# Kernel tuning notes

Measured on AMD Instinct MI355X. Metric: run time of the kernel, lower is better.

Reference implementation:

```python
import jax, jax.numpy as jnp
import numpy as np

B, T, D, H, STRIDE, MLP = 2, 2048, 1024, 16, 8, 4096
HD = D // H
EPS = 1e-5


def _ln(x, g, b):
    m = x.mean(-1, keepdims=True)
    v = x.var(-1, keepdims=True)
    return (x - m) * jax.lax.rsqrt(v + EPS) * g + b


def setup_inputs() -> dict:
    key = jax.random.key(0)
    ks = jax.random.split(key, 6)
    s = lambda k, shape: (jax.random.normal(k, shape, jnp.float32) * 0.02)
    return {
        "x": jax.random.normal(ks[0], (B, T, D), jnp.float32),
        "w_in": s(ks[1], (3 * D, D)),   # torch in_proj_weight
        "b_in": jnp.zeros((3 * D,), jnp.float32),
        "w_out": s(ks[2], (D, D)),      # attn out_proj
        "b_out": jnp.zeros((D,), jnp.float32),
        "w1": s(ks[3], (MLP, D)),       # mlp first Linear (torch layout [out,in])
        "b1": jnp.zeros((MLP,), jnp.float32),
        "w2": s(ks[4], (D, MLP)),       # mlp second Linear
        "b2": jnp.zeros((D,), jnp.float32),
        "ln1_g": jnp.ones((D,), jnp.float32),
        "ln1_b": jnp.zeros((D,), jnp.float32),
        "ln2_g": jnp.ones((D,), jnp.float32),
        "ln2_b": jnp.zeros((D,), jnp.float32),
    }


def reference(x, w_in, b_in, w_out, b_out, w1, b1, w2, b2,
              ln1_g, ln1_b, ln2_g, ln2_b):
    Bs, Ts, Ds = x.shape
    xn = _ln(x, ln1_g, ln1_b)
    # fused qkv projection (torch Linear: y = x @ W.T + b)
    qkv = xn @ w_in.T + b_in                              # [B,T,3D]
    q, k, v = jnp.split(qkv, 3, axis=-1)
    to_heads = lambda t: t.reshape(Bs, Ts, H, HD).transpose(0, 2, 1, 3)
    q, k, v = to_heads(q), to_heads(k), to_heads(v)       # [B,H,T,hd]
    scores = jnp.einsum("bhqd,bhkd->bhqk", q, k) / jnp.sqrt(jnp.float32(HD))
    # mask: rows at multiples of STRIDE attend everywhere; others only to self
    idx = jnp.arange(Ts)
    allowed = ((idx % STRIDE) == 0)[:, None] | (idx[:, None] == idx[None, :])
    scores = jnp.where(allowed, scores, -jnp.inf)
    attn = jax.nn.softmax(scores, axis=-1)
    o = jnp.einsum("bhqk,bhkd->bhqd", attn, v)            # [B,H,T,hd]
    o = o.transpose(0, 2, 1, 3).reshape(Bs, Ts, Ds)
    o = o @ w_out.T + b_out
    x = x + o
    xn = _ln(x, ln2_g, ln2_b)
    h = jax.nn.gelu(xn @ w1.T + b1, approximate=False)    # torch nn.GELU default = exact
    x = x + (h @ w2.T + b2)
    return x
```

## Files before the change

### kernel.cpp

```cpp
#include <hip/hip_runtime.h>

#define D_ 1024
#define T_ 2048
#define B_ 2
#define H_ 16
#define MLP_ 4096
#define NTOK (B_*T_)
#define QG 256
#define L2E 1.44269504088896340736f

typedef float f32x4 __attribute__((ext_vector_type(4)));
typedef __bf16 bf16x8 __attribute__((ext_vector_type(8)));

__device__ __forceinline__ unsigned short f2bf(float f) {
  unsigned int u = __float_as_uint(f);
  u += 0x7fff + ((u >> 16) & 1);
  return (unsigned short)(u >> 16);
}

__device__ __forceinline__ float wave_sum(float v) {
  for (int o = 32; o > 0; o >>= 1) v += __shfl_down(v, o, 64);
  return v;
}

__device__ __forceinline__ void gload16(const unsigned short* g, unsigned short* l) {
  __builtin_amdgcn_global_load_lds(
      (const __attribute__((address_space(1))) void*)g,
      (__attribute__((address_space(3))) void*)l, 16, 0, 0);
}

__device__ __forceinline__ unsigned ldsoff(const void* p) {
  return (unsigned)(size_t)(const __attribute__((address_space(3))) void*)p;
}

__device__ __forceinline__ void agload16(const unsigned short* g, unsigned m0v) {
  unsigned su = __builtin_amdgcn_readfirstlane(m0v);
  asm volatile("s_mov_b32 m0, %0\n\t"
               "global_load_lds_dwordx4 %1, off"
               :: "s"(su), "v"(g) : "memory");
}

#define N4_WIN  786432
#define N4_WOUT 262144
#define N4_W1   1048576
#define N4_W2   1048576
#define NCASTB  12288
__global__ void castln_kernel(const float* __restrict__ w_in,
                              const float* __restrict__ w_out,
                              const float* __restrict__ w1,
                              const float* __restrict__ w2,
                              unsigned short* __restrict__ o_in,
                              unsigned short* __restrict__ o_out,
                              unsigned short* __restrict__ o1,
                              unsigned short* __restrict__ o2,
                              const float* __restrict__ x,
                              const float* __restrict__ g,
                              const float* __restrict__ b,
                              unsigned short* __restrict__ xn) {
  int blk = blockIdx.x;
  int tid = threadIdx.x;
  if (blk < NTOK) {
    int wave = tid >> 6, lane = tid & 63;
    float4 v = ((const float4*)(x + (size_t)blk * D_))[tid];
    float s  = v.x + v.y + v.z + v.w;
    float s2 = v.x*v.x + v.y*v.y + v.z*v.z + v.w*v.w;
    s = wave_sum(s); s2 = wave_sum(s2);
    __shared__ float r1[4], r2[4];
    if (lane == 0) { r1[wave] = s; r2[wave] = s2; }
    __syncthreads();
    float ts  = r1[0] + r1[1] + r1[2] + r1[3];
    float ts2 = r2[0] + r2[1] + r2[2] + r2[3];
    float mean = ts * (1.0f / D_);
    float var  = ts2 * (1.0f / D_) - mean * mean;
    float rs = rsqrtf(var + 1e-5f);
    float4 gv = ((const float4*)g)[tid];
    float4 bv = ((const float4*)b)[tid];
    ushort4 o;
    o.x = f2bf((v.x - mean) * rs * gv.x + bv.x);
    o.y = f2bf((v.y - mean) * rs * gv.y + bv.y);
    o.z = f2bf((v.z - mean) * rs * gv.z + bv.z);
    o.w = f2bf((v.w - mean) * rs * gv.w + bv.w);
    ((ushort4*)(xn + (size_t)blk * D_))[tid] = o;
  } else {
    int i = (blk - NTOK) * 256 + tid;
    const float* src; unsigned short* dst; int j = i;
    if (i < N4_WIN) { src = w_in; dst = o_in; }
    else if ((j -= N4_WIN) < N4_WOUT) { src = w_out; dst = o_out; }
    else if ((j -= N4_WOUT) < N4_W1) { src = w1; dst = o1; }
    else { j -= N4_W1; src = w2; dst = o2; }
    float4 v = ((const float4*)src)[j];
    ushort4 o;
    o.x = f2bf(v.x); o.y = f2bf(v.y); o.z = f2bf(v.z); o.w = f2bf(v.w);
    ((ushort4*)dst)[j] = o;
  }
}

__global__ void ln_kernel(const float* __restrict__ x, const float* __restrict__ g,
                          const float* __restrict__ b, unsigned short* __restrict__ out) {
  int row = blockIdx.x;
  int tid = threadIdx.x;
  int wave = tid >> 6, lane = tid & 63;
  float4 v = ((const float4*)(x + (size_t)row * D_))[tid];
  float s  = v.x + v.y + v.z + v.w;
  float s2 = v.x*v.x + v.y*v.y + v.z*v.z + v.w*v.w;
  s = wave_sum(s); s2 = wave_sum(s2);
  __shared__ float r1[4], r2[4];
  if (lane == 0) { r1[wave] = s; r2[wave] = s2; }
  __syncthreads();
  float ts  = r1[0] + r1[1] + r1[2] + r1[3];
  float ts2 = r2[0] + r2[1] + r2[2] + r2[3];
  float mean = ts * (1.0f / D_);
  float var  = ts2 * (1.0f / D_) - mean * mean;
  float rs = rsqrtf(var + 1e-5f);
  float4 gv = ((const float4*)g)[tid];
  float4 bv = ((const float4*)b)[tid];
  ushort4 o;
  o.x = f2bf((v.x - mean) * rs * gv.x + bv.x);
  o.y = f2bf((v.y - mean) * rs * gv.y + bv.y);
  o.z = f2bf((v.z - mean) * rs * gv.z + bv.z);
  o.w = f2bf((v.w - mean) * rs * gv.w + bv.w);
  ((ushort4*)(out + (size_t)row * D_))[tid] = o;
}

__global__ void reduce_ln_kernel(const float* __restrict__ part,
                                 const float* __restrict__ x,
                                 const float* __restrict__ bias,
                                 const float* __restrict__ g,
                                 const float* __restrict__ b,
                                 float* __restrict__ x1,
                                 unsigned short* __restrict__ xn2) {
  int row = blockIdx.x;
  int tid = threadIdx.x;
  int wave = tid >> 6, lane = tid & 63;
  size_t base = (size_t)row * (D_ / 4) + tid;
  float4 v = ((const float4*)x)[base];
  float4 bo = ((const float4*)bias)[tid];
  v.x += bo.x; v.y += bo.y; v.z += bo.z; v.w += bo.w;
#pragma unroll
  for (int c = 0; c < 2; ++c) {
    float4 p = ((const float4*)part)[(size_t)c * (NTOK * (D_ / 4)) + base];
    v.x += p.x; v.y += p.y; v.z += p.z; v.w += p.w;
  }
  ((float4*)x1)[base] = v;
  float s  = v.x + v.y + v.z + v.w;
  float s2 = v.x*v.x + v.y*v.y + v.z*v.z + v.w*v.w;
  s = wave_sum(s); s2 = wave_sum(s2);
  __shared__ float r1[4], r2[4];
  if (lane == 0) { r1[wave] = s; r2[wave] = s2; }
  __syncthreads();
  float ts  = r1[0] + r1[1] + r1[2] + r1[3];
  float ts2 = r2[0] + r2[1] + r2[2] + r2[3];
  float mean = ts * (1.0f / D_);
  float var  = ts2 * (1.0f / D_) - mean * mean;
  float rs = rsqrtf(var + 1e-5f);
  float4 gv = ((const float4*)g)[tid];
  float4 bv = ((const float4*)b)[tid];
  ushort4 o;
  o.x = f2bf((v.x - mean) * rs * gv.x + bv.x);
  o.y = f2bf((v.y - mean) * rs * gv.y + bv.y);
  o.z = f2bf((v.z - mean) * rs * gv.z + bv.z);
  o.w = f2bf((v.w - mean) * rs * gv.w + bv.w);
  ((ushort4*)xn2)[base] = o;
}

__global__ void reduce_out_kernel(const float* __restrict__ part,
                                  const float* __restrict__ x1,
                                  const float* __restrict__ bias,
                                  float* __restrict__ out) {
  int i = blockIdx.x * 256 + threadIdx.x;
  float4 v = ((const float4*)x1)[i];
  float4 bo = ((const float4*)bias)[i & (D_ / 4 - 1)];
  v.x += bo.x; v.y += bo.y; v.z += bo.z; v.w += bo.w;
#pragma unroll
  for (int c = 0; c < 2; ++c) {
    float4 p = ((const float4*)part)[(size_t)c * (NTOK * (D_ / 4)) + i];
    v.x += p.x; v.y += p.y; v.z += p.z; v.w += p.w;
  }
  ((float4*)out)[i] = v;
}

template<int EPI>
__global__ __launch_bounds__(256)
void gemm128p_kernel(const unsigned short* __restrict__ A, int LDA,
                     const unsigned short* __restrict__ Bm, int LDB,
                     void* __restrict__ Cv, size_t sC, int LDC,
                     const float* __restrict__ bias,
                     unsigned short* __restrict__ aux1,
                     unsigned short* __restrict__ aux2,
                     int K, int nx, int ny) {
  __shared__ __align__(16) unsigned short As[2 * 8192];
  __shared__ __align__(16) unsigned short Bs[2 * 8192];
  const int flat = blockIdx.x;
  const int sxc = nx >> 1;
  const int nSuper = sxc * (ny >> 2);
  int s = flat % nSuper, pos = flat / nSuper;
  int sx = s % sxc, sy = s / sxc;
  const int bx = sx * 2 + (pos & 1);
  const int by = sy * 4 + (pos >> 1);
  const int m0 = by * 128, n0 = bx * 128;
  const int kOff = blockIdx.z * K;
  const int tid = threadIdx.x;
  const int lane = tid & 63, wave = tid >> 6;
  const int wm = (wave >> 1) * 64, wn = (wave & 1) * 64;
  const int fr = lane & 15, q = lane >> 4;
  const int f0 = ((q)     ^ (fr & 7)) << 3;
  const int f1 = ((4 + q) ^ (fr & 7)) << 3;

  const unsigned short* aS[4];
  const unsigned short* bS[4];
#pragma unroll
  for (int p = 0; p < 4; ++p) {
    int l = p * 256 + tid;
    int r = l >> 3;
    int cg = (l & 7) ^ (r & 7);
    aS[p] = A  + (size_t)(m0 + r) * LDA + kOff + cg * 8;
    bS[p] = Bm + (size_t)(n0 + r) * LDB + kOff + cg * 8;
  }
  const int NT = K >> 6;

  const unsigned aW = ldsoff(As) + wave * 1024;
  const unsigned bW = ldsoff(Bs) + wave * 1024;

#pragma unroll
  for (int p = 0; p < 4; ++p) {
    agload16(aS[p], aW + p * 4096);
    agload16(bS[p], bW + p * 4096);
  }
#pragma unroll
  for (int p = 0; p < 4; ++p) {
    agload16(aS[p] + 64, aW + 16384 + p * 4096);
    agload16(bS[p] + 64, bW + 16384 + p * 4096);
  }
  asm volatile("s_waitcnt vmcnt(8)");
  __builtin_amdgcn_sched_barrier(0);
  __builtin_amdgcn_s_barrier();

  f32x4 acc[4][4] = {};
  for (int t = 0; t < NT; ++t) {
    const int cb = (t & 1) << 13;
    const unsigned cbB = (t & 1) << 14;
    const unsigned short* Ab = As + cb;
    const unsigned short* Bb = Bs + cb;
    const int ko2 = (t + 2) << 6;
    {
      bf16x8 af[4], bfr[4];
#pragma unroll
      for (int i = 0; i < 4; ++i) af[i]  = *(const bf16x8*)&Ab[(wm + i * 16 + fr) * 64 + f0];
#pragma unroll
      for (int j = 0; j < 4; ++j) bfr[j] = *(const bf16x8*)&Bb[(wn + j * 16 + fr) * 64 + f0];
#pragma unroll
      for (int i = 0; i < 4; ++i)
#pragma unroll
        for (int j = 0; j < 4; ++j)
          acc[i][j] = __builtin_amdgcn_mfma_f32_16x16x32_bf16(af[i], bfr[j], acc[i][j], 0, 0, 0);
    }
    {
      bf16x8 af[4], bfr[4];
#pragma unroll
      for (int i = 0; i < 4; ++i) af[i]  = *(const bf16x8*)&Ab[(wm + i * 16 + fr) * 64 + f1];
#pragma unroll
      for (int j = 0; j < 4; ++j) bfr[j] = *(const bf16x8*)&Bb[(wn + j * 16 + fr) * 64 + f1];
#pragma unroll
      for (int i = 0; i < 4; ++i)
#pragma unroll
        for (int j = 0; j < 4; ++j)
          acc[i][j] = __builtin_amdgcn_mfma_f32_16x16x32_bf16(af[i], bfr[j], acc[i][j], 0, 0, 0);
    }
    __builtin_amdgcn_s_barrier();
    if (t + 2 < NT) {
#pragma unroll
      for (int p = 0; p < 4; ++p) {
        agload16(aS[p] + ko2, aW + cbB + p * 4096);
        agload16(bS[p] + ko2, bW + cbB + p * 4096);
      }
    }
    if (t + 1 < NT) {
      if (t + 2 < NT) asm volatile("s_waitcnt vmcnt(8)");
      else            asm volatile("s_waitcnt vmcnt(0)");
      __builtin_amdgcn_sched_barrier(0);
    }
    __builtin_amdgcn_s_barrier();
  }

  const int col = lane & 15, rbase = (lane >> 4) * 4;
#pragma unroll
  for (int i = 0; i < 4; ++i) {
#pragma unroll
    for (int j = 0; j < 4; ++j) {
      int gn = n0 + wn + j * 16 + col;
      int gmb = m0 + wm + i * 16 + rbase;
      float bv = (EPI == 2 || EPI == 8) ? bias[gn] : 0.0f;
#pragma unroll
      for (int r = 0; r < 4; ++r) {
        int gm = gmb + r;
        float v = acc[i][j][r] + bv;
        if (EPI == 2) {
          float u = v * (1.5957691216f + 0.0713548162f * v * v);
          float gl = v / (1.0f + exp2f(-L2E * u));
          ((unsigned short*)Cv)[(size_t)gm * LDC + gn] = f2bf(gl);
        } else if (EPI == 7) {
          ((float*)Cv)[(size_t)blockIdx.z * sC + (size_t)gm * LDC + gn] = v;
        } else {
          int sec = gn >> 10;
          int hh = (gn >> 6) & (H_ - 1);
          int dd = gn & 63;
          int t = gm & (T_ - 1);
          int b = gm >> 11;
          unsigned short bf = f2bf(v);
          if (sec == 0) {
            if (!(t & 7))
              aux1[(((size_t)(b * H_ + hh)) * QG + (t >> 3)) * 64 + dd] = bf;
          } else if (sec == 1) {
            aux2[(((size_t)(b * H_ + hh)) * T_ + t) * 64 + dd] = bf;
          } else {
            ((unsigned short*)Cv)[(size_t)gm * D_ + (gn - 2 * D_)] = bf;
          }
        }
      }
    }
  }
}

template<int EPI>
__global__ __launch_bounds__(512)
void gemm256a_kernel(const unsigned short* __restrict__ A, int LDA,
                     const unsigned short* __restrict__ Bm, int LDB,
                     void* __restrict__ Cv, size_t sC, int LDC,
                     const float* __restrict__ bias,
                     int K, int nx) {
  __shared__ __align__(16) unsigned short As[2 * 16384];
  __shared__ __align__(16) unsigned short Bs[2 * 16384];
  const int tid = threadIdx.x;
  const int lane = tid & 63, w = tid >> 6;
  const int wm = w >> 2, wn = w & 3;
  const int fr = lane & 15, q = lane >> 4, xr = fr & 7;

  const int nwg = gridDim.x;
  const int bid = blockIdx.x;
  const int l = (bid & 7) * (nwg >> 3) + (bid >> 3);
  const int bx = l % nx, by = l / nx;
  const int m0 = by * 256, n0 = bx * 256;
  const int kOff = blockIdx.z * K;

  const unsigned short* aS[4];
  const unsigned short* bS[4];
#pragma unroll
  for (int s = 0; s < 4; ++s) {
    int ls = s * 512 + tid;
    int r = ls >> 3;
    int cg = (ls & 7) ^ (r & 7);
    aS[s] = A  + (size_t)(m0 + r) * LDA + kOff + cg * 8;
    bS[s] = Bm + (size_t)(n0 + r) * LDB + kOff + cg * 8;
  }
  const int NT = K >> 6;

  const unsigned asb = ldsoff(As), bsb = ldsoff(Bs);
  const unsigned aW = asb + w * 1024, bW = bsb + w * 1024;

#pragma unroll
  for (int s = 0; s < 4; ++s) {
    agload16(aS[s], aW + s * 8192);
    agload16(bS[s], bW + s * 8192);
  }
#pragma unroll
  for (int s = 0; s < 4; ++s) {
    agload16(aS[s] + 64, aW + 32768 + s * 8192);
    agload16(bS[s] + 64, bW + 32768 + s * 8192);
  }
  asm volatile("s_waitcnt vmcnt(8)");
  __builtin_amdgcn_sched_barrier(0);
  __builtin_amdgcn_s_barrier();

  const int aOff = ((wm * 128 + fr) << 7) + ((q ^ xr) << 4);
  const int bOff = ((wn * 64 + fr) << 7) + ((q ^ xr) << 4);

  f32x4 acc[8][4] = {};

  for (int t = 0; t < NT; ++t) {
    const int cb = (t & 1) << 15;
    const char* Ab = (const char*)As + cb;
    const char* Bb = (const char*)Bs + cb;
    const unsigned aWc = aW + cb, bWc = bW + cb;
    const int ko2 = (t + 2) << 6;
    bf16x8 af[2][4], bfr[2][4];

#pragma unroll
    for (int i = 0; i < 4; ++i) {
      af[0][i] = *(const bf16x8*)(Ab + aOff + i * 2048);
      af[1][i] = *(const bf16x8*)(Ab + (aOff ^ 64) + i * 2048);
    }
#pragma unroll
    for (int j = 0; j < 2; ++j) {
      bfr[0][j] = *(const bf16x8*)(Bb + bOff + j * 2048);
      bfr[1][j] = *(const bf16x8*)(Bb + (bOff ^ 64) + j * 2048);
    }
    __builtin_amdgcn_s_barrier();
    __builtin_amdgcn_s_setprio(1);
#pragma unroll
    for (int i = 0; i < 4; ++i)
#pragma unroll
      for (int j = 0; j < 2; ++j) {
        acc[i][j] = __builtin_amdgcn_mfma_f32_16x16x32_bf16(af[0][i], bfr[0][j], acc[i][j], 0, 0, 0);
        acc[i][j] = __builtin_amdgcn_mfma_f32_16x16x32_bf16(af[1][i], bfr[1][j], acc[i][j], 0, 0, 0);
      }
    __builtin_amdgcn_s_setprio(0);
    __builtin_amdgcn_s_barrier();

#pragma unroll
    for (int j = 2; j < 4; ++j) {
      bfr[0][j] = *(const bf16x8*)(Bb + bOff + j * 2048);
      bfr[1][j] = *(const bf16x8*)(Bb + (bOff ^ 64) + j * 2048);
    }
    if (t + 2 < NT) {
      agload16(aS[0] + ko2, aWc);
      agload16(aS[2] + ko2, aWc + 16384);
    }
    __builtin_amdgcn_s_barrier();
    __builtin_amdgcn_s_setprio(1);
#pragma unroll
    for (int i = 0; i < 4; ++i)
#pragma unroll
      for (int j = 0; j < 2; ++j) {
        acc[i][2 + j] = __builtin_amdgcn_mfma_f32_16x16x32_bf16(af[0][i], bfr[0][2 + j], acc[i][2 + j], 0, 0, 0);
        acc[i][2 + j] = __builtin_amdgcn_mfma_f32_16x16x32_bf16(af[1][i], bfr[1][2 + j], acc[i][2 + j], 0, 0, 0);
      }
    __builtin_amdgcn_s_setprio(0);
    __builtin_amdgcn_s_barrier();

#pragma unroll
    for (int i = 0; i < 4; ++i) {
      af[0][i] = *(const bf16x8*)(Ab + (aOff + 8192) + i * 2048);
      af[1][i] = *(const bf16x8*)(Ab + ((aOff + 8192) ^ 64) + i * 2048);
    }
    if (t + 2 < NT) {
      agload16(bS[0] + ko2, bWc);
      agload16(bS[1] + ko2, bWc + 8192);
      agload16(bS[2] + ko2, bWc + 16384);
      agload16(bS[3] + ko2, bWc + 24576);
    }
    __builtin_amdgcn_s_barrier();
    __builtin_amdgcn_s_setprio(1);
#pragma unroll
    for (int i = 0; i < 4; ++i)
#pragma unroll
      for (int j = 0; j < 2; ++j) {
        acc[4 + i][j] = __builtin_amdgcn_mfma_f32_16x16x32_bf16(af[0][i], bfr[0][j], acc[4 + i][j], 0, 0, 0);
        acc[4 + i][j] = __builtin_amdgcn_mfma_f32_16x16x32_bf16(af[1][i], bfr[1][j], acc[4 + i][j], 0, 0, 0);
      }
    __builtin_amdgcn_s_setprio(0);
    __builtin_amdgcn_s_barrier();

    if (t + 2 < NT) {
      agload16(aS[1] + ko2, aWc + 8192);
      agload16(aS[3] + ko2, aWc + 24576);
    }
    if (t + 1 < NT) {
      if (t + 2 < NT) asm volatile("s_waitcnt vmcnt(8)");
      else            asm volatile("s_waitcnt vmcnt(0)");
      __builtin_amdgcn_sched_barrier(0);
    }
    __builtin_amdgcn_s_barrier();
    __builtin_amdgcn_s_setprio(1);
#pragma unroll
    for (int i = 0; i < 4; ++i)
#pragma unroll
      for (int j = 0; j < 2; ++j) {
        acc[4 + i][2 + j] = __builtin_amdgcn_mfma_f32_16x16x32_bf16(af[0][i], bfr[0][2 + j], acc[4 + i][2 + j], 0, 0, 0);
        acc[4 + i][2 + j] = __builtin_amdgcn_mfma_f32_16x16x32_bf16(af[1][i], bfr[1][2 + j], acc[4 + i][2 + j], 0, 0, 0);
      }
    __builtin_amdgcn_s_setprio(0);
    __builtin_amdgcn_s_barrier();
  }

  const int col = lane & 15, rbase = (lane >> 4) * 4;
  const int gm0 = m0 + wm * 128 + rbase;
  const int gn0 = n0 + wn * 64 + col;
#pragma unroll
  for (int mi = 0; mi < 8; ++mi) {
#pragma unroll
    for (int j = 0; j < 4; ++j) {
      int gn = gn0 + j * 16;
      float bv = (EPI == 2) ? bias[gn] : 0.0f;
#pragma unroll
      for (int r = 0; r < 4; ++r) {
        int gm = gm0 + mi * 16 + r;
        float v = acc[mi][j][r] + bv;
        if (EPI == 2) {
          float u = v * (1.5957691216f + 0.0713548162f * v * v);
          float gl = v / (1.0f + exp2f(-L2E * u));
          ((unsigned short*)Cv)[(size_t)gm * LDC + gn] = f2bf(gl);
        } else {
          ((float*)Cv)[(size_t)blockIdx.z * sC + (size_t)gm * LDC + gn] = v;
        }
      }
    }
  }
}

__global__ void vtrans_kernel(const unsigned short* __restrict__ vcomp,
                              unsigned short* __restrict__ Vt) {
  int blk = blockIdx.x;
  int tchunk = blk & 31;
  int bh = blk >> 5;
  int h = bh & (H_ - 1), b = bh >> 4;
  int t0 = tchunk * 64;
  __shared__ unsigned short ls[64][66];
  int tid = threadIdx.x;
#pragma unroll
  for (int it = 0; it < 16; ++it) {
    int linear = it * 256 + tid;
    int d = linear & 63, tl = linear >> 6;
    ls[d][tl] = vcomp[((size_t)(b * T_ + t0 + tl)) * D_ + h * 64 + d];
  }
  __syncthreads();
#pragma unroll
  for (int it = 0; it < 16; ++it) {
    int linear = it * 256 + tid;
    int tl = linear & 63, d = linear >> 6;
    Vt[((size_t)(bh * 64 + d)) * T_ + t0 + tl] = ls[d][tl];
  }
}

__global__ __launch_bounds__(256)
void flash_kernel(const unsigned short* __restrict__ Qg,
                  const unsigned short* __restrict__ Kh,
                  const unsigned short* __restrict__ Vt,
                  float* __restrict__ Opart,
                  float* __restrict__ ml) {
  const int kc = blockIdx.x, qt = blockIdx.y, bh = blockIdx.z;
  const int tid = threadIdx.x;
  const int lane = tid & 63, w = tid >> 6;
  const int fr = lane & 15, quad = lane >> 4;

  __shared__ __align__(16) unsigned short Qs[64 * 64];
  __shared__ __align__(16) unsigned short Ks[128 * 64];
  __shared__ __align__(16) unsigned short Vs[64 * 128];
  __shared__ __align__(16) unsigned short Ps[4 * 16 * 128];

  const unsigned short* Qbase = Qg + ((size_t)bh * 256 + qt * 64) * 64;
#pragma unroll
  for (int p = 0; p < 2; ++p) {
    int linear = p * 256 + tid;
    int r = linear >> 3, c = linear & 7;
    gload16(Qbase + r * 64 + (c ^ (r & 7)) * 8, &Qs[linear * 8]);
  }

  float m_run[4], l_run[4];
  f32x4 O[4] = {};
#pragma unroll
  for (int r = 0; r < 4; ++r) { m_run[r] = -3.0e38f; l_run[r] = 0.f; }

  const unsigned short* Kc = Kh + ((size_t)bh * T_ + kc * 512) * 64;
  const unsigned short* Vc = Vt + (size_t)bh * 64 * T_ + kc * 512;
  unsigned short* Pw = &Ps[w * 2048];
  const int arow = w * 16 + fr;

  for (int kt = 0; kt < 4; ++kt) {
    __syncthreads();
#pragma unroll
    for (int p = 0; p < 4; ++p) {
      int linear = p * 256 + tid;
      int r = linear >> 3, c = linear & 7;
      gload16(Kc + (size_t)(kt * 128 + r) * 64 + (c ^ (r & 7)) * 8, &Ks[linear * 8]);
    }
#pragma unroll
    for (int p = 0; p < 4; ++p) {
      int linear = p * 256 + tid;
      int r = linear >> 4, c = linear & 15;
      gload16(Vc + (size_t)r * T_ + kt * 128 + (c ^ (r & 7)) * 8, &Vs[linear * 8]);
    }
    __syncthreads();

    f32x4 s[8] = {};
    bf16x8 aq[2];
#pragma unroll
    for (int ks = 0; ks < 2; ++ks)
      aq[ks] = *(const bf16x8*)&Qs[arow * 64 + ((ks * 4 + quad) ^ (fr & 7)) * 8];
#pragma unroll
    for (int nf = 0; nf < 8; ++nf) {
      int krow = nf * 16 + fr;
#pragma unroll
      for (int ks = 0; ks < 2; ++ks) {
        bf16x8 bk = *(const bf16x8*)&Ks[krow * 64 + ((ks * 4 + quad) ^ (fr & 7)) * 8];
        s[nf] = __builtin_amdgcn_mfma_f32_16x16x32_bf16(aq[ks], bk, s[nf], 0, 0, 0);
      }
    }
    float alpha[4], rowsum[4];
#pragma unroll
    for (int r = 0; r < 4; ++r) {
      float mt = -3.0e38f;
#pragma unroll
      for (int nf = 0; nf < 8; ++nf) { s[nf][r] *= 0.125f; mt = fmaxf(mt, s[nf][r]); }
#pragma unroll
      for (int x = 1; x < 16; x <<= 1) mt = fmaxf(mt, __shfl_xor(mt, x, 64));
      float mn = fmaxf(m_run[r], mt);
      alpha[r] = exp2f((m_run[r] - mn) * L2E);
      m_run[r] = mn;
      rowsum[r] = 0.f;
    }
#pragma unroll
    for (int nf = 0; nf < 8; ++nf)
#pragma unroll
      for (int r = 0; r < 4; ++r) {
        float p = exp2f((s[nf][r] - m_run[r]) * L2E);
        s[nf][r] = p; rowsum[r] += p;
      }
#pragma unroll
    for (int r = 0; r < 4; ++r) {
#pragma unroll
      for (int x = 1; x < 16; x <<= 1) rowsum[r] += __shfl_xor(rowsum[r], x, 64);
      l_run[r] = l_run[r] * alpha[r] + rowsum[r];
    }
#pragma unroll
    for (int nf = 0; nf < 8; ++nf)
#pragma unroll
      for (int r = 0; r < 4; ++r) {
        int m = quad * 4 + r;
        int c = nf * 2 + (fr >> 3);
        Pw[m * 128 + ((c ^ (m & 7)) * 8) + (fr & 7)] = f2bf(s[nf][r]);
      }
#pragma unroll
    for (int nf2 = 0; nf2 < 4; ++nf2)
#pragma unroll
      for (int r = 0; r < 4; ++r) O[nf2][r] *= alpha[r];
#pragma unroll
    for (int ks2 = 0; ks2 < 4; ++ks2) {
      bf16x8 ap = *(const bf16x8*)&Pw[fr * 128 + (((ks2 * 4 + quad) ^ (fr & 7)) * 8)];
#pragma unroll
      for (int nf2 = 0; nf2 < 4; ++nf2) {
        int vrow = nf2 * 16 + fr;
        bf16x8 bv = *(const bf16x8*)&Vs[vrow * 128 + (((ks2 * 4 + quad) ^ (fr & 7)) * 8)];
        O[nf2] = __builtin_amdgcn_mfma_f32_16x16x32_bf16(ap, bv, O[nf2], 0, 0, 0);
      }
    }
  }

  int qbase = qt * 64 + w * 16;
  float* Ob = Opart + (((size_t)bh * 4 + kc) * 256 + qbase) * 64;
#pragma unroll
  for (int nf2 = 0; nf2 < 4; ++nf2)
#pragma unroll
    for (int r = 0; r < 4; ++r)
      Ob[(size_t)(quad * 4 + r) * 64 + nf2 * 16 + fr] = O[nf2][r];
  if (fr == 0) {
#pragma unroll
    for (int r = 0; r < 4; ++r) {
      size_t mi = ((((size_t)bh * 4 + kc) * 256) + qbase + quad * 4 + r) * 2;
      ml[mi] = m_run[r]; ml[mi + 1] = l_run[r];
    }
  }
}

__global__ void combine_kernel(const float* __restrict__ Opart,
                               const float* __restrict__ ml,
                               unsigned short* __restrict__ vcomp) {
  int idx = blockIdx.x * 256 + threadIdx.x;
  int c = idx & (D_ - 1);
  int qi = (idx >> 10) & (QG - 1);
  int b = idx >> 18;
  int h = c >> 6, d = c & 63;
  int bh = b * H_ + h;
  float m[4], l[4];
  float M = -3.0e38f;
#pragma unroll
  for (int ch = 0; ch < 4; ++ch) {
    size_t r = ((size_t)bh * 4 + ch) * 256 + qi;
    m[ch] = ml[r * 2]; l[ch] = ml[r * 2 + 1];
    M = fmaxf(M, m[ch]);
  }
  float osum = 0.f, lsum = 0.f;
#pragma unroll
  for (int ch = 0; ch < 4; ++ch) {
    size_t r = ((size_t)bh * 4 + ch) * 256 + qi;
    float wgt = exp2f((m[ch] - M) * L2E);
    osum += wgt * Opart[r * 64 + d];
    lsum += wgt * l[ch];
  }
  vcomp[((size_t)(b * T_ + qi * 8)) * D_ + c] = f2bf(osum / lsum);
}

extern "C" void kernel_launch(void* const* d_in, const int* in_sizes, int n_in,
                              void* d_out, int out_size, void* d_ws, size_t ws_size,
                              hipStream_t stream) {
  const float* x     = (const float*)d_in[0];
  const float* w_in  = (const float*)d_in[1];
  const float* b_in  = (const float*)d_in[2];
  const float* w_out = (const float*)d_in[3];
  const float* b_out = (const float*)d_in[4];
  const float* w1    = (const float*)d_in[5];
  const float* b1    = (const float*)d_in[6];
  const float* w2    = (const float*)d_in[7];
  const float* b2    = (const float*)d_in[8];
  const float* ln1_g = (const float*)d_in[9];
  const float* ln1_b = (const float*)d_in[10];
  const float* ln2_g = (const float*)d_in[11];
  const float* ln2_b = (const float*)d_in[12];
  float* out = (float*)d_out;

  char* ws = (char*)d_ws;
  size_t off = 0;
  auto alloc = [&](size_t bytes) -> void* {
    void* p = ws + off;
    off += (bytes + 255) & ~(size_t)255;
    return p;
  };
  unsigned short* w_inb = (unsigned short*)alloc((size_t)3 * D_ * D_ * 2);
  unsigned short* w_outb= (unsigned short*)alloc((size_t)D_ * D_ * 2);
  unsigned short* w1b   = (unsigned short*)alloc((size_t)MLP_ * D_ * 2);
  unsigned short* w2b   = (unsigned short*)alloc((size_t)D_ * MLP_ * 2);
  unsigned short* vcomp = (unsigned short*)alloc((size_t)NTOK * D_ * 2);
  float*          x1    = (float*)         alloc((size_t)NTOK * D_ * 4);
  unsigned short* xn2   = (unsigned short*)alloc((size_t)NTOK * D_ * 2);
  unsigned short* h     = (unsigned short*)alloc((size_t)NTOK * MLP_ * 2);
  char* U = (char*)alloc((size_t)40 * 1024 * 1024);
  float*          P2    = (float*)U;
  unsigned short* xn    = (unsigned short*)U;
  unsigned short* Qg    = (unsigned short*)(U + 8388608);
  unsigned short* Kh    = (unsigned short*)(U + 12582912);
  unsigned short* Vt    = (unsigned short*)(U + 20971520);
  float*          Opart = (float*)         (U + 29360128);
  float*          mlbuf = (float*)         (U + 37748736);

  castln_kernel<<<NTOK + NCASTB, 256, 0, stream>>>(
      w_in, w_out, w1, w2, w_inb, w_outb, w1b, w2b, x, ln1_g, ln1_b, xn);

  gemm128p_kernel<8><<<dim3(24 * 32, 1, 1), 256, 0, stream>>>(
      xn, D_, w_inb, D_, vcomp, 0, 3 * D_, b_in, Qg, Kh, 1024, 24, 32);

  vtrans_kernel<<<1024, 256, 0, stream>>>(vcomp, Vt);

  flash_kernel<<<dim3(4, 4, 32), 256, 0, stream>>>(Qg, Kh, Vt, Opart, mlbuf);

  combine_kernel<<<2048, 256, 0, stream>>>(Opart, mlbuf, vcomp);

  gemm128p_kernel<7><<<dim3(8 * 32, 1, 2), 256, 0, stream>>>(
      vcomp, D_, w_outb, D_, P2, (size_t)NTOK * D_, D_, nullptr, nullptr, nullptr,
      512, 8, 32);

  reduce_ln_kernel<<<NTOK, 256, 0, stream>>>(P2, x, b_out, ln2_g, ln2_b, x1, xn2);

  gemm256a_kernel<2><<<dim3(256, 1, 1), 512, 0, stream>>>(
      xn2, D_, w1b, D_, h, 0, MLP_, b1, 1024, 16);

  gemm128p_kernel<7><<<dim3(8 * 32, 1, 2), 256, 0, stream>>>(
      h, MLP_, w2b, MLP_, P2, (size_t)NTOK * D_, D_, nullptr, nullptr, nullptr,
      2048, 8, 32);

  reduce_out_kernel<<<4096, 256, 0, stream>>>(P2, x1, b2, out);
}
```

Before: 313.8 us.

## Use new 128x256-tile 512-thread GEMM for QKV projection with scatter epilogue

Adds a gemm256b kernel that computes 128x256 output tiles with 8 waves and a double-buffered K=32 pipeline, and uses it for the QKV projection with the head-scatter epilogue. The old 128x128 gemm128p path is stripped of its QKV-specific epilogue arguments, and the unused ln_kernel is removed. Larger N tiles raise operand reuse and halve the block count to 384. The cost is a shorter K step per barrier and more registers per thread.

```diff
diff --git a/kernel.cpp b/kernel.cpp
--- a/kernel.cpp
+++ b/kernel.cpp
@@ -95,33 +95,6 @@
   }
 }
 
-__global__ void ln_kernel(const float* __restrict__ x, const float* __restrict__ g,
-                          const float* __restrict__ b, unsigned short* __restrict__ out) {
-  int row = blockIdx.x;
-  int tid = threadIdx.x;
-  int wave = tid >> 6, lane = tid & 63;
-  float4 v = ((const float4*)(x + (size_t)row * D_))[tid];
-  float s  = v.x + v.y + v.z + v.w;
-  float s2 = v.x*v.x + v.y*v.y + v.z*v.z + v.w*v.w;
-  s = wave_sum(s); s2 = wave_sum(s2);
-  __shared__ float r1[4], r2[4];
-  if (lane == 0) { r1[wave] = s; r2[wave] = s2; }
-  __syncthreads();
-  float ts  = r1[0] + r1[1] + r1[2] + r1[3];
-  float ts2 = r2[0] + r2[1] + r2[2] + r2[3];
-  float mean = ts * (1.0f / D_);
-  float var  = ts2 * (1.0f / D_) - mean * mean;
-  float rs = rsqrtf(var + 1e-5f);
-  float4 gv = ((const float4*)g)[tid];
-  float4 bv = ((const float4*)b)[tid];
-  ushort4 o;
-  o.x = f2bf((v.x - mean) * rs * gv.x + bv.x);
-  o.y = f2bf((v.y - mean) * rs * gv.y + bv.y);
-  o.z = f2bf((v.z - mean) * rs * gv.z + bv.z);
-  o.w = f2bf((v.w - mean) * rs * gv.w + bv.w);
-  ((ushort4*)(out + (size_t)row * D_))[tid] = o;
-}
-
 __global__ void reduce_ln_kernel(const float* __restrict__ part,
                                  const float* __restrict__ x,
                                  const float* __restrict__ bias,
@@ -185,8 +158,6 @@
                      const unsigned short* __restrict__ Bm, int LDB,
                      void* __restrict__ Cv, size_t sC, int LDC,
                      const float* __restrict__ bias,
-                     unsigned short* __restrict__ aux1,
-                     unsigned short* __restrict__ aux2,
                      int K, int nx, int ny) {
   __shared__ __align__(16) unsigned short As[2 * 8192];
   __shared__ __align__(16) unsigned short Bs[2 * 8192];
@@ -289,7 +260,7 @@
     for (int j = 0; j < 4; ++j) {
       int gn = n0 + wn + j * 16 + col;
       int gmb = m0 + wm + i * 16 + rbase;
-      float bv = (EPI == 2 || EPI == 8) ? bias[gn] : 0.0f;
+      float bv = (EPI == 2) ? bias[gn] : 0.0f;
 #pragma unroll
       for (int r = 0; r < 4; ++r) {
         int gm = gmb + r;
@@ -298,8 +269,285 @@
           float u = v * (1.5957691216f + 0.0713548162f * v * v);
           float gl = v / (1.0f + exp2f(-L2E * u));
           ((unsigned short*)Cv)[(size_t)gm * LDC + gn] = f2bf(gl);
-        } else if (EPI == 7) {
+        } else {
           ((float*)Cv)[(size_t)blockIdx.z * sC + (size_t)gm * LDC + gn] = v;
+        }
+      }
+    }
+  }
+}
+
+template<int EPI>
+__global__ __launch_bounds__(512)
+void gemm256a_kernel(const unsigned short* __restrict__ A, int LDA,
+                     const unsigned short* __restrict__ Bm, int LDB,
+                     void* __restrict__ Cv, size_t sC, int LDC,
+                     const float* __restrict__ bias,
+                     int K, int nx) {
+  __shared__ __align__(16) unsigned short As[2 * 16384];
+  __shared__ __align__(16) unsigned short Bs[2 * 16384];
+  const int tid = threadIdx.x;
+  const int lane = tid & 63, w = tid >> 6;
+  const int wm = w >> 2, wn = w & 3;
+  const int fr = lane & 15, q = lane >> 4, xr = fr & 7;
+
+  const int nwg = gridDim.x;
+  const int bid = blockIdx.x;
+  const int l = (bid & 7) * (nwg >> 3) + (bid >> 3);
+  const int bx = l % nx, by = l / nx;
+  const int m0 = by * 256, n0 = bx * 256;
+  const int kOff = blockIdx.z * K;
+
+  const unsigned short* aS[4];
+  const unsigned short* bS[4];
+#pragma unroll
+  for (int s = 0; s < 4; ++s) {
+    int ls = s * 512 + tid;
+    int r = ls >> 3;
+    int cg = (ls & 7) ^ (r & 7);
+    aS[s] = A  + (size_t)(m0 + r) * LDA + kOff + cg * 8;
+    bS[s] = Bm + (size_t)(n0 + r) * LDB + kOff + cg * 8;
+  }
+  const int NT = K >> 6;
+
+  const unsigned asb = ldsoff(As), bsb = ldsoff(Bs);
+  const unsigned aW = asb + w * 1024, bW = bsb + w * 1024;
+
+#pragma unroll
+  for (int s = 0; s < 4; ++s) {
+    agload16(aS[s], aW + s * 8192);
+    agload16(bS[s], bW + s * 8192);
+  }
+#pragma unroll
+  for (int s = 0; s < 4; ++s) {
+    agload16(aS[s] + 64, aW + 32768 + s * 8192);
+    agload16(bS[s] + 64, bW + 32768 + s * 8192);
+  }
+  asm volatile("s_waitcnt vmcnt(8)");
+  __builtin_amdgcn_sched_barrier(0);
+  __builtin_amdgcn_s_barrier();
+
+  const int aOff = ((wm * 128 + fr) << 7) + ((q ^ xr) << 4);
+  const int bOff = ((wn * 64 + fr) << 7) + ((q ^ xr) << 4);
+
+  f32x4 acc[8][4] = {};
+
+  for (int t = 0; t < NT; ++t) {
+    const int cb = (t & 1) << 15;
+    const char* Ab = (const char*)As + cb;
+    const char* Bb = (const char*)Bs + cb;
+    const unsigned aWc = aW + cb, bWc = bW + cb;
+    const int ko2 = (t + 2) << 6;
+    bf16x8 af[2][4], bfr[2][4];
+
+#pragma unroll
+    for (int i = 0; i < 4; ++i) {
+      af[0][i] = *(const bf16x8*)(Ab + aOff + i * 2048);
+      af[1][i] = *(const bf16x8*)(Ab + (aOff ^ 64) + i * 2048);
+    }
+#pragma unroll
+    for (int j = 0; j < 2; ++j) {
+      bfr[0][j] = *(const bf16x8*)(Bb + bOff + j * 2048);
+      bfr[1][j] = *(const bf16x8*)(Bb + (bOff ^ 64) + j * 2048);
+    }
+    __builtin_amdgcn_s_barrier();
+    __builtin_amdgcn_s_setprio(1);
+#pragma unroll
+    for (int i = 0; i < 4; ++i)
+#pragma unroll
+      for (int j = 0; j < 2; ++j) {
+        acc[i][j] = __builtin_amdgcn_mfma_f32_16x16x32_bf16(af[0][i], bfr[0][j], acc[i][j], 0, 0, 0);
+        acc[i][j] = __builtin_amdgcn_mfma_f32_16x16x32_bf16(af[1][i], bfr[1][j], acc[i][j], 0, 0, 0);
+      }
+    __builtin_amdgcn_s_setprio(0);
+    __builtin_amdgcn_s_barrier();
+
+#pragma unroll
+    for (int j = 2; j < 4; ++j) {
+      bfr[0][j] = *(const bf16x8*)(Bb + bOff + j * 2048);
+      bfr[1][j] = *(const bf16x8*)(Bb + (bOff ^ 64) + j * 2048);
+    }
+    if (t + 2 < NT) {
+      agload16(aS[0] + ko2, aWc);
+      agload16(aS[2] + ko2, aWc + 16384);
+    }
+    __builtin_amdgcn_s_barrier();
+    __builtin_amdgcn_s_setprio(1);
+#pragma unroll
+    for (int i = 0; i < 4; ++i)
+#pragma unroll
+      for (int j = 0; j < 2; ++j) {
+        acc[i][2 + j] = __builtin_amdgcn_mfma_f32_16x16x32_bf16(af[0][i], bfr[0][2 + j], acc[i][2 + j], 0, 0, 0);
+        acc[i][2 + j] = __builtin_amdgcn_mfma_f32_16x16x32_bf16(af[1][i], bfr[1][2 + j], acc[i][2 + j], 0, 0, 0);
+      }
+    __builtin_amdgcn_s_setprio(0);
+    __builtin_amdgcn_s_barrier();
+
+#pragma unroll
+    for (int i = 0; i < 4; ++i) {
+      af[0][i] = *(const bf16x8*)(Ab + (aOff + 8192) + i * 2048);
+      af[1][i] = *(const bf16x8*)(Ab + ((aOff + 8192) ^ 64) + i * 2048);
+    }
+    if (t + 2 < NT) {
+      agload16(bS[0] + ko2, bWc);
+      agload16(bS[1] + ko2, bWc + 8192);
+      agload16(bS[2] + ko2, bWc + 16384);
+      agload16(bS[3] + ko2, bWc + 24576);
+    }
+    __builtin_amdgcn_s_barrier();
+    __builtin_amdgcn_s_setprio(1);
+#pragma unroll
+    for (int i = 0; i < 4; ++i)
+#pragma unroll
+      for (int j = 0; j < 2; ++j) {
+        acc[4 + i][j] = __builtin_amdgcn_mfma_f32_16x16x32_bf16(af[0][i], bfr[0][j], acc[4 + i][j], 0, 0, 0);
+        acc[4 + i][j] = __builtin_amdgcn_mfma_f32_16x16x32_bf16(af[1][i], bfr[1][j], acc[4 + i][j], 0, 0, 0);
+      }
+    __builtin_amdgcn_s_setprio(0);
+    __builtin_amdgcn_s_barrier();
+
+    if (t + 2 < NT) {
+      agload16(aS[1] + ko2, aWc + 8192);
+      agload16(aS[3] + ko2, aWc + 24576);
+    }
+    if (t + 1 < NT) {
+      if (t + 2 < NT) asm volatile("s_waitcnt vmcnt(8)");
+      else            asm volatile("s_waitcnt vmcnt(0)");
+      __builtin_amdgcn_sched_barrier(0);
+    }
+    __builtin_amdgcn_s_barrier();
+    __builtin_amdgcn_s_setprio(1);
+#pragma unroll
+    for (int i = 0; i < 4; ++i)
+#pragma unroll
+      for (int j = 0; j < 2; ++j) {
+        acc[4 + i][2 + j] = __builtin_amdgcn_mfma_f32_16x16x32_bf16(af[0][i], bfr[0][2 + j], acc[4 + i][2 + j], 0, 0, 0);
+        acc[4 + i][2 + j] = __builtin_amdgcn_mfma_f32_16x16x32_bf16(af[1][i], bfr[1][2 + j], acc[4 + i][2 + j], 0, 0, 0);
+      }
+    __builtin_amdgcn_s_setprio(0);
+    __builtin_amdgcn_s_barrier();
+  }
+
+  const int col = lane & 15, rbase = (lane >> 4) * 4;
+  const int gm0 = m0 + wm * 128 + rbase;
+  const int gn0 = n0 + wn * 64 + col;
+#pragma unroll
+  for (int mi = 0; mi < 8; ++mi) {
+#pragma unroll
+    for (int j = 0; j < 4; ++j) {
+      int gn = gn0 + j * 16;
+      float bv = (EPI == 2) ? bias[gn] : 0.0f;
+#pragma unroll
+      for (int r = 0; r < 4; ++r) {
+        int gm = gm0 + mi * 16 + r;
+        float v = acc[mi][j][r] + bv;
+        if (EPI == 2) {
+          float u = v * (1.5957691216f + 0.0713548162f * v * v);
+          float gl = v / (1.0f + exp2f(-L2E * u));
+          ((unsigned short*)Cv)[(size_t)gm * LDC + gn] = f2bf(gl);
+        } else {
+          ((float*)Cv)[(size_t)blockIdx.z * sC + (size_t)gm * LDC + gn] = v;
+        }
+      }
+    }
+  }
+}
+
+template<int EPI>
+__global__ __launch_bounds__(512)
+void gemm256b_kernel(const unsigned short* __restrict__ A, int LDA,
+                     const unsigned short* __restrict__ Bm, int LDB,
+                     unsigned short* __restrict__ Cv, int LDC,
+                     const float* __restrict__ bias,
+                     unsigned short* __restrict__ aux1,
+                     unsigned short* __restrict__ aux2,
+                     int K, int nx) {
+  __shared__ __align__(16) unsigned short As[2 * 4096];
+  __shared__ __align__(16) unsigned short Bs[2 * 8192];
+  const int tid = threadIdx.x;
+  const int lane = tid & 63, wv = tid >> 6;
+  const int wm = (wv >> 2) * 64, wn = (wv & 3) * 64;
+  const int fr = lane & 15, q = lane >> 4;
+
+  const int nwg = gridDim.x;
+  const int bid = blockIdx.x;
+  const int l = (bid & 7) * (nwg >> 3) + (bid >> 3);
+  const int bx = l % nx, by = l / nx;
+  const int m0 = by * 128, n0 = bx * 256;
+
+  const int rA = tid >> 2, sA = tid & 3;
+  const int cA = sA ^ ((rA >> 1) & 3);
+  const unsigned short* aSrc = A  + (size_t)(m0 + rA) * LDA + cA * 8;
+  const unsigned short* bSrc0 = Bm + (size_t)(n0 + rA) * LDB + cA * 8;
+  const unsigned short* bSrc1 = Bm + (size_t)(n0 + 128 + rA) * LDB + cA * 8;
+  const int NT = K >> 5;
+
+  const unsigned aWb = ldsoff(As) + wv * 1024;
+  const unsigned bWb = ldsoff(Bs) + wv * 1024;
+
+  agload16(aSrc, aWb);
+  agload16(bSrc0, bWb);
+  agload16(bSrc1, bWb + 8192);
+  agload16(aSrc + 32, aWb + 8192);
+  agload16(bSrc0 + 32, bWb + 16384);
+  agload16(bSrc1 + 32, bWb + 24576);
+  asm volatile("s_waitcnt vmcnt(3)");
+  __builtin_amdgcn_sched_barrier(0);
+  __builtin_amdgcn_s_barrier();
+
+  f32x4 acc[4][4] = {};
+  for (int t = 0; t < NT; ++t) {
+    const unsigned cbA = (t & 1) ? 8192u : 0u;
+    const unsigned cbB = (t & 1) ? 16384u : 0u;
+    const char* Ab = (const char*)As + cbA;
+    const char* Bb = (const char*)Bs + cbB;
+    const int ko2 = (t + 2) << 5;
+    bf16x8 af[4], bfr[4];
+#pragma unroll
+    for (int i = 0; i < 4; ++i) {
+      int ra = wm + i * 16 + fr;
+      af[i] = *(const bf16x8*)(Ab + ra * 64 + ((q ^ ((ra >> 1) & 3)) << 4));
+    }
+#pragma unroll
+    for (int j = 0; j < 4; ++j) {
+      int rb = wn + j * 16 + fr;
+      bfr[j] = *(const bf16x8*)(Bb + rb * 64 + ((q ^ ((rb >> 1) & 3)) << 4));
+    }
+#pragma unroll
+    for (int i = 0; i < 4; ++i)
+#pragma unroll
+      for (int j = 0; j < 4; ++j)
+        acc[i][j] = __builtin_amdgcn_mfma_f32_16x16x32_bf16(af[i], bfr[j], acc[i][j], 0, 0, 0);
+    __builtin_amdgcn_s_barrier();
+    if (t + 2 < NT) {
+      agload16(aSrc + ko2, aWb + cbA);
+      agload16(bSrc0 + ko2, bWb + cbB);
+      agload16(bSrc1 + ko2, bWb + cbB + 8192);
+    }
+    if (t + 1 < NT) {
+      if (t + 2 < NT) asm volatile("s_waitcnt vmcnt(3)");
+      else            asm volatile("s_waitcnt vmcnt(0)");
+      __builtin_amdgcn_sched_barrier(0);
+    }
+    __builtin_amdgcn_s_barrier();
+  }
+
+  const int col = lane & 15, rbase = (lane >> 4) * 4;
+#pragma unroll
+  for (int i = 0; i < 4; ++i) {
+#pragma unroll
+    for (int j = 0; j < 4; ++j) {
+      int gn = n0 + wn + j * 16 + col;
+      int gmb = m0 + wm + i * 16 + rbase;
+      float bv = bias[gn];
+#pragma unroll
+      for (int r = 0; r < 4; ++r) {
+        int gm = gmb + r;
+        float v = acc[i][j][r] + bv;
+        if (EPI == 2) {
+          float u = v * (1.5957691216f + 0.0713548162f * v * v);
+          float gl = v / (1.0f + exp2f(-L2E * u));
+          Cv[(size_t)gm * LDC + gn] = f2bf(gl);
         } else {
           int sec = gn >> 10;
           int hh = (gn >> 6) & (H_ - 1);
@@ -313,184 +561,8 @@
           } else if (sec == 1) {
             aux2[(((size_t)(b * H_ + hh)) * T_ + t) * 64 + dd] = bf;
           } else {
-            ((unsigned short*)Cv)[(size_t)gm * D_ + (gn - 2 * D_)] = bf;
+            Cv[(size_t)gm * D_ + (gn - 2 * D_)] = bf;
           }
-        }
-      }
-    }
-  }
-}
-
-template<int EPI>
-__global__ __launch_bounds__(512)
-void gemm256a_kernel(const unsigned short* __restrict__ A, int LDA,
-                     const unsigned short* __restrict__ Bm, int LDB,
-                     void* __restrict__ Cv, size_t sC, int LDC,
-                     const float* __restrict__ bias,
-                     int K, int nx) {
-  __shared__ __align__(16) unsigned short As[2 * 16384];
-  __shared__ __align__(16) unsigned short Bs[2 * 16384];
-  const int tid = threadIdx.x;
-  const int lane = tid & 63, w = tid >> 6;
-  const int wm = w >> 2, wn = w & 3;
-  const int fr = lane & 15, q = lane >> 4, xr = fr & 7;
-
-  const int nwg = gridDim.x;
-  const int bid = blockIdx.x;
-  const int l = (bid & 7) * (nwg >> 3) + (bid >> 3);
-  const int bx = l % nx, by = l / nx;
-  const int m0 = by * 256, n0 = bx * 256;
-  const int kOff = blockIdx.z * K;
-
-  const unsigned short* aS[4];
-  const unsigned short* bS[4];
-#pragma unroll
-  for (int s = 0; s < 4; ++s) {
-    int ls = s * 512 + tid;
-    int r = ls >> 3;
-    int cg = (ls & 7) ^ (r & 7);
-    aS[s] = A  + (size_t)(m0 + r) * LDA + kOff + cg * 8;
-    bS[s] = Bm + (size_t)(n0 + r) * LDB + kOff + cg * 8;
-  }
-  const int NT = K >> 6;
-
-  const unsigned asb = ldsoff(As), bsb = ldsoff(Bs);
-  const unsigned aW = asb + w * 1024, bW = bsb + w * 1024;
-
-#pragma unroll
-  for (int s = 0; s < 4; ++s) {
-    agload16(aS[s], aW + s * 8192);
-    agload16(bS[s], bW + s * 8192);
-  }
-#pragma unroll
-  for (int s = 0; s < 4; ++s) {
-    agload16(aS[s] + 64, aW + 32768 + s * 8192);
-    agload16(bS[s] + 64, bW + 32768 + s * 8192);
-  }
-  asm volatile("s_waitcnt vmcnt(8)");
-  __builtin_amdgcn_sched_barrier(0);
-  __builtin_amdgcn_s_barrier();
-
-  const int aOff = ((wm * 128 + fr) << 7) + ((q ^ xr) << 4);
-  const int bOff = ((wn * 64 + fr) << 7) + ((q ^ xr) << 4);
-
-  f32x4 acc[8][4] = {};
-
-  for (int t = 0; t < NT; ++t) {
-    const int cb = (t & 1) << 15;
-    const char* Ab = (const char*)As + cb;
-    const char* Bb = (const char*)Bs + cb;
-    const unsigned aWc = aW + cb, bWc = bW + cb;
-    const int ko2 = (t + 2) << 6;
-    bf16x8 af[2][4], bfr[2][4];
-
-#pragma unroll
-    for (int i = 0; i < 4; ++i) {
-      af[0][i] = *(const bf16x8*)(Ab + aOff + i * 2048);
-      af[1][i] = *(const bf16x8*)(Ab + (aOff ^ 64) + i * 2048);
-    }
-#pragma unroll
-    for (int j = 0; j < 2; ++j) {
-      bfr[0][j] = *(const bf16x8*)(Bb + bOff + j * 2048);
-      bfr[1][j] = *(const bf16x8*)(Bb + (bOff ^ 64) + j * 2048);
-    }
-    __builtin_amdgcn_s_barrier();
-    __builtin_amdgcn_s_setprio(1);
-#pragma unroll
-    for (int i = 0; i < 4; ++i)
-#pragma unroll
-      for (int j = 0; j < 2; ++j) {
-        acc[i][j] = __builtin_amdgcn_mfma_f32_16x16x32_bf16(af[0][i], bfr[0][j], acc[i][j], 0, 0, 0);
-        acc[i][j] = __builtin_amdgcn_mfma_f32_16x16x32_bf16(af[1][i], bfr[1][j], acc[i][j], 0, 0, 0);
-      }
-    __builtin_amdgcn_s_setprio(0);
-    __builtin_amdgcn_s_barrier();
-
-#pragma unroll
-    for (int j = 2; j < 4; ++j) {
-      bfr[0][j] = *(const bf16x8*)(Bb + bOff + j * 2048);
-      bfr[1][j] = *(const bf16x8*)(Bb + (bOff ^ 64) + j * 2048);
-    }
-    if (t + 2 < NT) {
-      agload16(aS[0] + ko2, aWc);
-      agload16(aS[2] + ko2, aWc + 16384);
-    }
-    __builtin_amdgcn_s_barrier();
-    __builtin_amdgcn_s_setprio(1);
-#pragma unroll
-    for (int i = 0; i < 4; ++i)
-#pragma unroll
-      for (int j = 0; j < 2; ++j) {
-        acc[i][2 + j] = __builtin_amdgcn_mfma_f32_16x16x32_bf16(af[0][i], bfr[0][2 + j], acc[i][2 + j], 0, 0, 0);
-        acc[i][2 + j] = __builtin_amdgcn_mfma_f32_16x16x32_bf16(af[1][i], bfr[1][2 + j], acc[i][2 + j], 0, 0, 0);
-      }
-    __builtin_amdgcn_s_setprio(0);
-    __builtin_amdgcn_s_barrier();
-
-#pragma unroll
-    for (int i = 0; i < 4; ++i) {
-      af[0][i] = *(const bf16x8*)(Ab + (aOff + 8192) + i * 2048);
-      af[1][i] = *(const bf16x8*)(Ab + ((aOff + 8192) ^ 64) + i * 2048);
-    }
-    if (t + 2 < NT) {
-      agload16(bS[0] + ko2, bWc);
-      agload16(bS[1] + ko2, bWc + 8192);
-      agload16(bS[2] + ko2, bWc + 16384);
-      agload16(bS[3] + ko2, bWc + 24576);
-    }
-    __builtin_amdgcn_s_barrier();
-    __builtin_amdgcn_s_setprio(1);
-#pragma unroll
-    for (int i = 0; i < 4; ++i)
-#pragma unroll
-      for (int j = 0; j < 2; ++j) {
-        acc[4 + i][j] = __builtin_amdgcn_mfma_f32_16x16x32_bf16(af[0][i], bfr[0][j], acc[4 + i][j], 0, 0, 0);
-        acc[4 + i][j] = __builtin_amdgcn_mfma_f32_16x16x32_bf16(af[1][i], bfr[1][j], acc[4 + i][j], 0, 0, 0);
-      }
-    __builtin_amdgcn_s_setprio(0);
-    __builtin_amdgcn_s_barrier();
-
-    if (t + 2 < NT) {
-      agload16(aS[1] + ko2, aWc + 8192);
-      agload16(aS[3] + ko2, aWc + 24576);
-    }
-    if (t + 1 < NT) {
-      if (t + 2 < NT) asm volatile("s_waitcnt vmcnt(8)");
-      else            asm volatile("s_waitcnt vmcnt(0)");
-      __builtin_amdgcn_sched_barrier(0);
-    }
-    __builtin_amdgcn_s_barrier();
-    __builtin_amdgcn_s_setprio(1);
-#pragma unroll
-    for (int i = 0; i < 4; ++i)
-#pragma unroll
-      for (int j = 0; j < 2; ++j) {
-        acc[4 + i][2 + j] = __builtin_amdgcn_mfma_f32_16x16x32_bf16(af[0][i], bfr[0][2 + j], acc[4 + i][2 + j], 0, 0, 0);
-        acc[4 + i][2 + j] = __builtin_amdgcn_mfma_f32_16x16x32_bf16(af[1][i], bfr[1][2 + j], acc[4 + i][2 + j], 0, 0, 0);
-      }
-    __builtin_amdgcn_s_setprio(0);
-    __builtin_amdgcn_s_barrier();
-  }
-
-  const int col = lane & 15, rbase = (lane >> 4) * 4;
-  const int gm0 = m0 + wm * 128 + rbase;
-  const int gn0 = n0 + wn * 64 + col;
-#pragma unroll
-  for (int mi = 0; mi < 8; ++mi) {
-#pragma unroll
-    for (int j = 0; j < 4; ++j) {
-      int gn = gn0 + j * 16;
-      float bv = (EPI == 2) ? bias[gn] : 0.0f;
-#pragma unroll
-      for (int r = 0; r < 4; ++r) {
-        int gm = gm0 + mi * 16 + r;
-        float v = acc[mi][j][r] + bv;
-        if (EPI == 2) {
-          float u = v * (1.5957691216f + 0.0713548162f * v * v);
-          float gl = v / (1.0f + exp2f(-L2E * u));
-          ((unsigned short*)Cv)[(size_t)gm * LDC + gn] = f2bf(gl);
-        } else {
-          ((float*)Cv)[(size_t)blockIdx.z * sC + (size_t)gm * LDC + gn] = v;
         }
       }
     }
@@ -724,8 +796,8 @@
   castln_kernel<<<NTOK + NCASTB, 256, 0, stream>>>(
       w_in, w_out, w1, w2, w_inb, w_outb, w1b, w2b, x, ln1_g, ln1_b, xn);
 
-  gemm128p_kernel<8><<<dim3(24 * 32, 1, 1), 256, 0, stream>>>(
-      xn, D_, w_inb, D_, vcomp, 0, 3 * D_, b_in, Qg, Kh, 1024, 24, 32);
+  gemm256b_kernel<8><<<dim3(384, 1, 1), 512, 0, stream>>>(
+      xn, D_, w_inb, D_, vcomp, 3 * D_, b_in, Qg, Kh, 1024, 12);
 
   vtrans_kernel<<<1024, 256, 0, stream>>>(vcomp, Vt);
 
@@ -734,7 +806,7 @@
   combine_kernel<<<2048, 256, 0, stream>>>(Opart, mlbuf, vcomp);
 
   gemm128p_kernel<7><<<dim3(8 * 32, 1, 2), 256, 0, stream>>>(
-      vcomp, D_, w_outb, D_, P2, (size_t)NTOK * D_, D_, nullptr, nullptr, nullptr,
+      vcomp, D_, w_outb, D_, P2, (size_t)NTOK * D_, D_, nullptr,
       512, 8, 32);
 
   reduce_ln_kernel<<<NTOK, 256, 0, stream>>>(P2, x, b_out, ln2_g, ln2_b, x1, xn2);
@@ -743,7 +815,7 @@
       xn2, D_, w1b, D_, h, 0, MLP_, b1, 1024, 16);
 
   gemm128p_kernel<7><<<dim3(8 * 32, 1, 2), 256, 0, stream>>>(
-      h, MLP_, w2b, MLP_, P2, (size_t)NTOK * D_, D_, nullptr, nullptr, nullptr,
+      h, MLP_, w2b, MLP_, P2, (size_t)NTOK * D_, D_, nullptr,
       2048, 8, 32);
 
   reduce_out_kernel<<<4096, 256, 0, stream>>>(P2, x1, b2, out);
```

New measurement: 314.2 us. About the same (+0.1%).
